# Performance work log

Hardware: AMD Instinct MI355X
Metric: run time of the kernel (lower is better)

The kernel has to match this reference:

```python
import jax, jax.numpy as jnp
import numpy as np

N, T, F_DIM, E = 50000, 64, 64, 800000


def setup_inputs() -> dict:
    key = jax.random.key(0)
    k1, k2, k3, k4 = jax.random.split(key, 4)
    company_tensor = jax.random.normal(k1, (N, T, F_DIM), dtype=jnp.float32)
    edge_index = jax.random.randint(k2, (2, E), 0, N, dtype=jnp.int32)
    # GCNConv weight (glorot-ish scale) and bias
    W = jax.random.normal(k3, (F_DIM, F_DIM), dtype=jnp.float32) * (1.0 / np.sqrt(F_DIM))
    b = jax.random.normal(k4, (F_DIM,), dtype=jnp.float32) * 0.02
    return {"company_tensor": company_tensor, "edge_index": edge_index, "W": W, "b": b}


def reference(company_tensor, edge_index, W, b):
    # PyG GCNConv with self-loops and symmetric normalization, applied per timestep, then ReLU.
    src, dst = edge_index[0], edge_index[1]
    # degree including self-loops (computed once; fixed graph across T)
    deg = jax.ops.segment_sum(jnp.ones((E,), dtype=company_tensor.dtype), dst, num_segments=N) + 1.0
    dis = jax.lax.rsqrt(deg)                       # deg >= 1, no inf handling needed
    norm = dis[src] * dis[dst]                     # [E] edge weights
    self_norm = (dis * dis)[:, None]               # [N,1] self-loop weight = 1/deg
    # Linear transform for all timesteps at once: [N,T,F] x [F,F] -> [T,N,F]
    xw = jnp.einsum('ntf,fg->tng', company_tensor, W)

    def step(_, xw_t):
        # gather messages from src, scale, scatter-add into dst
        agg = jax.ops.segment_sum(norm[:, None] * xw_t[src], dst, num_segments=N)
        out_t = jax.nn.relu(agg + self_norm * xw_t + b)
        return None, out_t

    _, out = jax.lax.scan(step, None, xw)          # [T,N,F]
    return jnp.transpose(out, (1, 0, 2))           # [N,T,F]
```

## Files before the change

kernel.cpp:

```cpp
#include <hip/hip_runtime.h>

#define NN 50000
#define TT 64
#define FF 64
#define EE 800000

typedef __attribute__((ext_vector_type(4))) float f32x4;
typedef __attribute__((ext_vector_type(8))) short bf16x8;

__device__ __forceinline__ unsigned short f2bf(float x) {
  unsigned int u = __float_as_uint(x);
  u = (u + 0x7FFFu + ((u >> 16) & 1u)) >> 16;
  return (unsigned short)u;
}
__device__ __forceinline__ float bf2f(unsigned short h) {
  return __uint_as_float(((unsigned int)h) << 16);
}


__global__ void k_count(const int* __restrict__ dst, int* __restrict__ cnt) {
  int e = blockIdx.x * 256 + threadIdx.x;
  if (e < EE) atomicAdd(&cnt[dst[e]], 1);
}

__global__ void k_dis(const int* __restrict__ cnt, float* __restrict__ dis) {
  int n = blockIdx.x * 256 + threadIdx.x;
  if (n < NN) dis[n] = rsqrtf((float)(cnt[n] + 1));
}

__global__ void k_scan(const int* __restrict__ cnt, int* __restrict__ off) {
  __shared__ int s[1024];
  __shared__ int carry;
  int tid = threadIdx.x;
  if (tid == 0) carry = 0;
  __syncthreads();
  for (int base = 0; base < NN; base += 1024) {
    int i = base + tid;
    int v = (i < NN) ? (cnt[i] + 1) : 0;
    s[tid] = v;
    __syncthreads();
    for (int d = 1; d < 1024; d <<= 1) {
      int x = (tid >= d) ? s[tid - d] : 0;
      __syncthreads();
      s[tid] += x;
      __syncthreads();
    }
    if (i < NN) off[i] = carry + s[tid] - v;
    __syncthreads();
    if (tid == 0) carry += s[1023];
    __syncthreads();
  }
  if (tid == 0) off[NN] = carry;
}

__global__ void k_self(const int* __restrict__ off, const float* __restrict__ dis,
                       int2* __restrict__ edges, int* __restrict__ fill) {
  int n = blockIdx.x * 256 + threadIdx.x;
  if (n < NN) {
    float d = dis[n];
    edges[off[n]] = make_int2(n, __float_as_int(d * d));
    fill[n] = 1;
  }
}

__global__ void k_fill(const int* __restrict__ src, const int* __restrict__ dst,
                       const int* __restrict__ off, const float* __restrict__ dis,
                       int* __restrict__ fill, int2* __restrict__ edges) {
  int e = blockIdx.x * 256 + threadIdx.x;
  if (e < EE) {
    int s = src[e], d = dst[e];
    int pos = off[d] + atomicAdd(&fill[d], 1);
    edges[pos] = make_int2(s, __float_as_int(dis[s] * dis[d]));
  }
}

__global__ __launch_bounds__(256) void k_gemm(const float* __restrict__ X,
                                              const float* __restrict__ W,
                                              unsigned short* __restrict__ Y) {
  __shared__ unsigned short Wt[64 * 72];
  int tid = threadIdx.x;
#pragma unroll
  for (int i = 0; i < 16; ++i) {
    int idx = i * 256 + tid;
    int f = idx >> 6, g = idx & 63;
    Wt[g * 72 + f] = f2bf(W[idx]);
  }
  __syncthreads();
  int wv = tid >> 6;
  int lane = tid & 63;
  int n = blockIdx.x * 4 + wv;
  int m16 = lane & 15, q = lane >> 4;
  const float* Xn = X + (size_t)n * 4096;

  bf16x8 afr[4][2];
#pragma unroll
  for (int mt = 0; mt < 4; ++mt)
#pragma unroll
    for (int kt = 0; kt < 2; ++kt) {
      const float* p = Xn + (mt * 16 + m16) * 64 + kt * 32 + q * 8;
      f32x4 lo = *(const f32x4*)p;
      f32x4 hi = *(const f32x4*)(p + 4);
      bf16x8 fr;
      fr[0] = (short)f2bf(lo[0]); fr[1] = (short)f2bf(lo[1]);
      fr[2] = (short)f2bf(lo[2]); fr[3] = (short)f2bf(lo[3]);
      fr[4] = (short)f2bf(hi[0]); fr[5] = (short)f2bf(hi[1]);
      fr[6] = (short)f2bf(hi[2]); fr[7] = (short)f2bf(hi[3]);
      afr[mt][kt] = fr;
    }
  bf16x8 bfr[4][2];
#pragma unroll
  for (int nt = 0; nt < 4; ++nt)
#pragma unroll
    for (int kt = 0; kt < 2; ++kt)
      bfr[nt][kt] = *(const bf16x8*)&Wt[(nt * 16 + m16) * 72 + kt * 32 + q * 8];

  f32x4 acc[4][4];
#pragma unroll
  for (int mt = 0; mt < 4; ++mt)
#pragma unroll
    for (int nt = 0; nt < 4; ++nt)
      acc[mt][nt] = (f32x4){0.f, 0.f, 0.f, 0.f};

#pragma unroll
  for (int kt = 0; kt < 2; ++kt)
#pragma unroll
    for (int mt = 0; mt < 4; ++mt)
#pragma unroll
      for (int nt = 0; nt < 4; ++nt)
        acc[mt][nt] = __builtin_amdgcn_mfma_f32_16x16x32_bf16(
            bfr[nt][kt], afr[mt][kt], acc[mt][nt], 0, 0, 0);

#pragma unroll
  for (int mt = 0; mt < 4; ++mt) {
    int t = mt * 16 + m16;
#pragma unroll
    for (int nt = 0; nt < 4; ++nt) {
      int g = nt * 16 + q * 4;
      ushort4 pk;
      pk.x = f2bf(acc[mt][nt][0]);
      pk.y = f2bf(acc[mt][nt][1]);
      pk.z = f2bf(acc[mt][nt][2]);
      pk.w = f2bf(acc[mt][nt][3]);
      *(ushort4*)(Y + ((size_t)t * NN + n) * 64 + g) = pk;
    }
  }
}

__global__ __launch_bounds__(256) void k_agg(const unsigned short* __restrict__ Y,
                                             const int2* __restrict__ edges,
                                             const int* __restrict__ off,
                                             const float* __restrict__ bias,
                                             float* __restrict__ out) {
  int wv = threadIdx.x >> 6;
  int lane = threadIdx.x & 63;
  int n = blockIdx.x * 4 + wv;
  int t = blockIdx.y;
  int q = lane >> 4, fq = (lane & 15) * 4;
  const unsigned short* Yt = Y + (size_t)t * (NN * 64);
  int start = off[n], end = off[n + 1];
  float a0 = 0.f, a1 = 0.f, a2 = 0.f, a3 = 0.f;
  for (int i = start + q; i < end; i += 4) {
    int2 e = edges[i];
    float w = __int_as_float(e.y);
    ushort4 yv = *(const ushort4*)(Yt + e.x * 64 + fq);
    a0 += w * bf2f(yv.x);
    a1 += w * bf2f(yv.y);
    a2 += w * bf2f(yv.z);
    a3 += w * bf2f(yv.w);
  }
  a0 += __shfl_xor(a0, 16, 64); a0 += __shfl_xor(a0, 32, 64);
  a1 += __shfl_xor(a1, 16, 64); a1 += __shfl_xor(a1, 32, 64);
  a2 += __shfl_xor(a2, 16, 64); a2 += __shfl_xor(a2, 32, 64);
  a3 += __shfl_xor(a3, 16, 64); a3 += __shfl_xor(a3, 32, 64);
  if (q == 0) {
    f32x4 bb = *(const f32x4*)(bias + fq);
    f32x4 r;
    r[0] = fmaxf(a0 + bb[0], 0.f);
    r[1] = fmaxf(a1 + bb[1], 0.f);
    r[2] = fmaxf(a2 + bb[2], 0.f);
    r[3] = fmaxf(a3 + bb[3], 0.f);
    *(f32x4*)(out + ((size_t)n * TT + t) * 64 + fq) = r;
  }
}


extern "C" void kernel_launch(void* const* d_in, const int* in_sizes, int n_in,
                              void* d_out, int out_size, void* d_ws, size_t ws_size,
                              hipStream_t stream) {
  const float* X = (const float*)d_in[0];
  const int* ei = (const int*)d_in[1];
  const float* W = (const float*)d_in[2];
  const float* b = (const float*)d_in[3];
  float* out = (float*)d_out;

  char* ws = (char*)d_ws;
  unsigned short* Y = (unsigned short*)ws;
  int2* edges = (int2*)(ws + 409600000ULL);
  int* cnt  = (int*)(ws + 416400000ULL);
  int* off  = (int*)(ws + 416600000ULL);
  int* fill = (int*)(ws + 416800008ULL);
  float* dis = (float*)(ws + 417000008ULL);

  hipMemsetAsync(cnt, 0, NN * sizeof(int), stream);

  k_count<<<(EE + 255) / 256, 256, 0, stream>>>(ei + EE, cnt);
  k_dis<<<(NN + 255) / 256, 256, 0, stream>>>(cnt, dis);
  k_scan<<<1, 1024, 0, stream>>>(cnt, off);
  k_self<<<(NN + 255) / 256, 256, 0, stream>>>(off, dis, edges, fill);
  k_fill<<<(EE + 255) / 256, 256, 0, stream>>>(ei, ei + EE, off, dis, fill, edges);
  k_gemm<<<NN / 4, 256, 0, stream>>>(X, W, Y);
  k_agg<<<dim3(NN / 4, TT), 256, 0, stream>>>(Y, edges, off, b, out);
}
```

Measured before the change: 3.273 ms.

## Store XW node-major and aggregate all timesteps per node in one wave

The intermediate XW buffer moves from [T,N,F] to [N,T,F] layout, so each neighbor's full 8KB row across all timesteps is contiguous. The aggregation kernel now has each wave handle one node for all 64 timesteps, walking the edge list once instead of 64 times and issuing wide contiguous gathers per neighbor. It also prefetches the next edge and writes the output in contiguous node-major rows. In exchange, each lane keeps a 64-float accumulator, which raises register pressure, and parallelism drops to one wave per node, so edges are processed serially within a wave.

```diff
diff --git a/kernel.cpp b/kernel.cpp
--- a/kernel.cpp
+++ b/kernel.cpp
@@ -130,6 +130,7 @@
         acc[mt][nt] = __builtin_amdgcn_mfma_f32_16x16x32_bf16(
             bfr[nt][kt], afr[mt][kt], acc[mt][nt], 0, 0, 0);
 
+  unsigned short* Yn = Y + (size_t)n * 4096;
 #pragma unroll
   for (int mt = 0; mt < 4; ++mt) {
     int t = mt * 16 + m16;
@@ -141,7 +142,7 @@
       pk.y = f2bf(acc[mt][nt][1]);
       pk.z = f2bf(acc[mt][nt][2]);
       pk.w = f2bf(acc[mt][nt][3]);
-      *(ushort4*)(Y + ((size_t)t * NN + n) * 64 + g) = pk;
+      *(ushort4*)(Yn + t * 64 + g) = pk;
     }
   }
 }
@@ -154,32 +155,49 @@
   int wv = threadIdx.x >> 6;
   int lane = threadIdx.x & 63;
   int n = blockIdx.x * 4 + wv;
-  int t = blockIdx.y;
-  int q = lane >> 4, fq = (lane & 15) * 4;
-  const unsigned short* Yt = Y + (size_t)t * (NN * 64);
+  int fc = lane & 7;
+  int tr = lane >> 3;
   int start = off[n], end = off[n + 1];
-  float a0 = 0.f, a1 = 0.f, a2 = 0.f, a3 = 0.f;
-  for (int i = start + q; i < end; i += 4) {
-    int2 e = edges[i];
+
+  float acc[8][8];
+#pragma unroll
+  for (int k = 0; k < 8; ++k)
+#pragma unroll
+    for (int j = 0; j < 8; ++j) acc[k][j] = 0.f;
+
+  int laneoff = tr * 64 + fc * 8;
+
+  int2 e = edges[start];
+  for (int i = start; i < end; ++i) {
+    int inext = i + 1;
+    int2 en = (inext < end) ? edges[inext] : e;
     float w = __int_as_float(e.y);
-    ushort4 yv = *(const ushort4*)(Yt + e.x * 64 + fq);
-    a0 += w * bf2f(yv.x);
-    a1 += w * bf2f(yv.y);
-    a2 += w * bf2f(yv.z);
-    a3 += w * bf2f(yv.w);
-  }
-  a0 += __shfl_xor(a0, 16, 64); a0 += __shfl_xor(a0, 32, 64);
-  a1 += __shfl_xor(a1, 16, 64); a1 += __shfl_xor(a1, 32, 64);
-  a2 += __shfl_xor(a2, 16, 64); a2 += __shfl_xor(a2, 32, 64);
-  a3 += __shfl_xor(a3, 16, 64); a3 += __shfl_xor(a3, 32, 64);
-  if (q == 0) {
-    f32x4 bb = *(const f32x4*)(bias + fq);
-    f32x4 r;
-    r[0] = fmaxf(a0 + bb[0], 0.f);
-    r[1] = fmaxf(a1 + bb[1], 0.f);
-    r[2] = fmaxf(a2 + bb[2], 0.f);
-    r[3] = fmaxf(a3 + bb[3], 0.f);
-    *(f32x4*)(out + ((size_t)n * TT + t) * 64 + fq) = r;
+    const unsigned short* row = Y + (size_t)e.x * 4096 + laneoff;
+#pragma unroll
+    for (int k = 0; k < 8; ++k) {
+      bf16x8 v = *(const bf16x8*)(row + k * 512);
+#pragma unroll
+      for (int j = 0; j < 8; ++j)
+        acc[k][j] += w * bf2f((unsigned short)v[j]);
+    }
+    e = en;
+  }
+
+  float bb[8];
+#pragma unroll
+  for (int j = 0; j < 8; ++j) bb[j] = bias[fc * 8 + j];
+
+  float* outp = out + (size_t)n * 4096 + laneoff;
+#pragma unroll
+  for (int k = 0; k < 8; ++k) {
+    f32x4 r0, r1;
+#pragma unroll
+    for (int j = 0; j < 4; ++j) {
+      r0[j] = fmaxf(acc[k][j] + bb[j], 0.f);
+      r1[j] = fmaxf(acc[k][j + 4] + bb[j + 4], 0.f);
+    }
+    *(f32x4*)(outp + k * 512) = r0;
+    *(f32x4*)(outp + k * 512 + 4) = r1;
   }
 }
 
@@ -209,5 +227,5 @@
   k_self<<<(NN + 255) / 256, 256, 0, stream>>>(off, dis, edges, fill);
   k_fill<<<(EE + 255) / 256, 256, 0, stream>>>(ei, ei + EE, off, dis, fill, edges);
   k_gemm<<<NN / 4, 256, 0, stream>>>(X, W, Y);
-  k_agg<<<dim3(NN / 4, TT), 256, 0, stream>>>(Y, edges, off, b, out);
-}
+  k_agg<<<dim3(NN / 4, 1), 256, 0, stream>>>(Y, edges, off, b, out);
+}
```

Result: faster. 2.649 ms (-19.1%).
